# Kernel tuning notes

Measured on AMD Instinct MI355X. Metric: run time of the kernel, lower is better.

The kernel has to match this reference:

```python
import jax, jax.numpy as jnp
import numpy as np

N = 64      # SSM state size (hidden_size)
H = 1024    # channels
L = 2048    # sequence length
BATCH = 8


def setup_inputs() -> dict:
    key = jax.random.key(0)
    ks = jax.random.split(key, 12)
    s = 1.0 / np.sqrt(N)
    n = jnp.arange(N, dtype=jnp.float32)
    return {
        "r": jax.random.normal(ks[0], (BATCH, L, H), dtype=jnp.float32),
        "B_re": jax.random.normal(ks[1], (N,), dtype=jnp.float32) * s,
        "B_im": jax.random.normal(ks[2], (N,), dtype=jnp.float32) * s,
        "C_re": jax.random.normal(ks[3], (H, N), dtype=jnp.float32) * s,
        "C_im": jax.random.normal(ks[4], (H, N), dtype=jnp.float32) * s,
        "P_re": jax.random.normal(ks[5], (N,), dtype=jnp.float32) * s,
        "P_im": jax.random.normal(ks[6], (N,), dtype=jnp.float32) * s,
        "Q_re": jax.random.normal(ks[7], (N,), dtype=jnp.float32) * s,
        "Q_im": jax.random.normal(ks[8], (N,), dtype=jnp.float32) * s,
        # HiPPO-LegS-like diagonal: negative real part for stability, imag ~ pi*n
        "diag_re": -0.5 * jnp.ones((N,), dtype=jnp.float32),
        "diag_im": jnp.pi * (n - N / 2.0),
        "step": jnp.array([1e-3], dtype=jnp.float32),
        "D": jnp.zeros((1,), dtype=jnp.float32),
    }


def _dplr_kernel(Bc, Cc, Pc, Qc, Lam, step, seq_len):
    # Standard S4 DPLR generating function evaluated at roots of unity,
    # then inverse FFT -> real convolution kernel K_c of shape (H, L).
    z = jnp.exp(-2j * jnp.pi * jnp.arange(seq_len) / seq_len).astype(jnp.complex64)  # (L,)
    g = (2.0 / step) * (1.0 - z) / (1.0 + z)                                          # (L,)
    cden = 1.0 / (g[:, None] - Lam[None, :])                                          # (L,N) Cauchy denom
    k00 = jnp.einsum('hn,ln->hl', Cc * Bc, cden)   # (H,L)
    k01 = jnp.einsum('hn,ln->hl', Cc * Pc, cden)   # (H,L)
    k10 = jnp.einsum('n,ln->l', Qc * Bc, cden)     # (L,)
    k11 = jnp.einsum('n,ln->l', Qc * Pc, cden)     # (L,)
    at_roots = (2.0 / (1.0 + z)) * (k00 - k01 * (k10 / (1.0 + k11)))  # (H,L)
    return jnp.fft.ifft(at_roots, axis=-1).real


def reference(r, B_re, B_im, C_re, C_im, P_re, P_im, Q_re, Q_im,
              diag_re, diag_im, step, D):
    step_c = jnp.maximum(step[0], 1e-6)
    Bc = B_re + 1j * B_im
    Cc = C_re + 1j * C_im
    Pc = P_re + 1j * P_im
    Qc = Q_re + 1j * Q_im
    Lam = diag_re + 1j * diag_im
    seq_len = r.shape[1]
    K = _dplr_kernel(Bc, Cc, Pc, Qc, Lam, step_c, seq_len)  # (H, L)
    # causal FFT convolution along the sequence axis
    nfft = 2 * seq_len
    Kf = jnp.fft.rfft(K, n=nfft, axis=-1)            # (H, nfft//2+1)
    uf = jnp.fft.rfft(r, n=nfft, axis=1)             # (B, nfft//2+1, H)
    h1 = jnp.fft.irfft(uf * Kf.T[None], n=nfft, axis=1)[:, :seq_len]  # (B,L,H)
    y1 = h1 + D[0] * r
    return jax.nn.gelu(y1, approximate=False)
```

## Files before the change

kernel.cpp:

```cpp
#include <hip/hip_runtime.h>
#include <math.h>

#define SSM_N 64
#define SSM_H 1024
#define SSM_L 2048
#define SSM_B 8
#define FFTN 2048
#define NT 256
#define KFS 2052

#define PSWZ(a) ((a) ^ (((a) >> 4) & 15))

typedef float f2 __attribute__((ext_vector_type(2)));
static __device__ __forceinline__ f2 mkf2(float a, float b){ f2 v; v.x = a; v.y = b; return v; }

static __device__ __forceinline__ f2 cmul(f2 a, f2 b){
  return mkf2(-a.y, a.y) * mkf2(b.y, b.x) + mkf2(a.x, a.x) * b;
}
static __device__ __forceinline__ f2 cconj(f2 a){ return mkf2(a.x, -a.y); }

template<bool INV> static __device__ __forceinline__ f2 mul_mi(f2 a){
  return INV ? mkf2(-a.y, a.x) : mkf2(a.y, -a.x);
}
template<bool INV> static __device__ __forceinline__ f2 mul_w81(f2 a){
  const float r = 0.70710678118654752440f;
  return INV ? (r * mkf2(a.x - a.y, a.y + a.x)) : (r * mkf2(a.x + a.y, a.y - a.x));
}
template<bool INV> static __device__ __forceinline__ f2 mul_w83(f2 a){
  const float r = 0.70710678118654752440f;
  return INV ? (r * mkf2(-(a.x + a.y), a.x - a.y)) : (r * mkf2(a.y - a.x, -(a.x + a.y)));
}

template<bool INV>
static __device__ __forceinline__ void bfly8_store(f2* __restrict__ dst, const f2* __restrict__ tw,
                                                   f2* x, int j, int base, int S)
{
  f2 t0=x[0]+x[4], t4=x[0]-x[4];
  f2 t1=x[1]+x[5], t5=x[1]-x[5];
  f2 t2=x[2]+x[6], t6=x[2]-x[6];
  f2 t3=x[3]+x[7], t7=x[3]-x[7];
  f2 b0=t0+t2, b2=t0-t2, b1=t1+t3, b3=t1-t3;
  f2 mb3 = mul_mi<INV>(b3);
  f2 y0=b0+b1, y4=b0-b1, y2=b2+mb3, y6=b2-mb3;
  f2 v1 = mul_w81<INV>(t5), v2 = mul_mi<INV>(t6), v3 = mul_w83<INV>(t7);
  f2 a0=t4+v2, a2=t4-v2, a1=v1+v3, a3=v1-v3;
  f2 ma3 = mul_mi<INV>(a3);
  f2 y1=a0+a1, y5=a0-a1, y3=a2+ma3, y7=a2-ma3;
  f2 w1 = tw[j];
  if (INV) w1.y = -w1.y;
  f2 w2 = cmul(w1,w1);
  f2 w3 = cmul(w2,w1);
  f2 w4 = cmul(w2,w2);
  f2 w5 = cmul(w3,w2);
  f2 w6 = cmul(w3,w3);
  f2 w7 = cmul(w4,w3);
  dst[PSWZ(base)]     = y0;
  dst[PSWZ(base+S)]   = cmul(y1,w1);
  dst[PSWZ(base+2*S)] = cmul(y2,w2);
  dst[PSWZ(base+3*S)] = cmul(y3,w3);
  dst[PSWZ(base+4*S)] = cmul(y4,w4);
  dst[PSWZ(base+5*S)] = cmul(y5,w5);
  dst[PSWZ(base+6*S)] = cmul(y6,w6);
  dst[PSWZ(base+7*S)] = cmul(y7,w7);
}

template<bool INV, bool ZTOP>
static __device__ __forceinline__ void stage8_first(const f2* __restrict__ src, f2* __restrict__ dst,
                                                    const f2* __restrict__ tw, int t, int st)
{
  const f2* sp = src + st;
  f2 x[8];
  if (ZTOP) {
    #pragma unroll
    for (int q = 0; q < 4; ++q) { x[q] = sp[256*q]; x[q+4] = x[q]; }
    #pragma unroll
    for (int q = 0; q < 4; ++q) x[q+4] = mkf2(0.f, 0.f);
  } else {
    #pragma unroll
    for (int q = 0; q < 8; ++q) x[q] = sp[256*q];
  }
  bfly8_store<INV>(dst, tw, x, t, t*8, 1);
}

template<bool INV, int S>
static __device__ __forceinline__ void stage8_mid(const f2* __restrict__ src, f2* __restrict__ dst,
                                                  const f2* __restrict__ tw, int t, int st)
{
  const f2* sp = src + st;
  f2 x[8];
  #pragma unroll
  for (int q = 0; q < 8; ++q) x[q] = sp[256*q];
  int i = t & (S-1);
  int j = t - i;
  bfly8_store<INV>(dst, tw, x, j, i + j*8, S);
}

template<bool INV, bool HALFOUT>
static __device__ __forceinline__ void stage4f(const f2* __restrict__ src, f2* __restrict__ dst, int st)
{
  #pragma unroll
  for (int hh = 0; hh < 2; ++hh) {
    const f2* sp = src + st + 256*hh;
    f2* wp = dst + st + 256*hh;
    f2 x0=sp[0], x1=sp[512], x2=sp[1024], x3=sp[1536];
    f2 a0=x0+x2, a2=x0-x2, a1=x1+x3, a3=x1-x3;
    f2 m = mul_mi<INV>(a3);
    wp[0]   = a0+a1;
    wp[512] = a2+m;
    if (!HALFOUT) {
      wp[1024] = a0-a1;
      wp[1536] = a2-m;
    }
  }
}

template<bool INV, bool ZTOP, bool HALFOUT>
static __device__ void fft2048(f2* A, f2* B, const f2* tw, int t, int st)
{
  __syncthreads();
  stage8_first<INV, ZTOP>(A, B, tw, t, st);
  __syncthreads();
  stage8_mid<INV, 8>(B, A, tw, t, st);
  __syncthreads();
  stage8_mid<INV, 64>(A, B, tw, t, st);
  __syncthreads();
  stage4f<INV, HALFOUT>(B, A, st);
  __syncthreads();
}

static __device__ __forceinline__ void init_tw(f2* tw, int t)
{
  float s, c;
  sincosf(-6.2831853071795864769f * (float)t / (float)FFTN, &s, &c);
  tw[t] = mkf2(c, s);
}

__global__ __launch_bounds__(256) void kernel_cden(
    const float* __restrict__ B_re, const float* __restrict__ B_im,
    const float* __restrict__ P_re, const float* __restrict__ P_im,
    const float* __restrict__ Q_re, const float* __restrict__ Q_im,
    const float* __restrict__ diag_re, const float* __restrict__ diag_im,
    const float* __restrict__ step,
    f2* __restrict__ cdenT, f2* __restrict__ f2v, f2* __restrict__ facv)
{
  int l = blockIdx.x * blockDim.x + threadIdx.x;
  if (l >= SSM_L) return;
  double stepc = (double)step[0]; if (stepc < 1e-6) stepc = 1e-6;
  double ang = -2.0 * 3.14159265358979323846 * (double)l / (double)SSM_L;
  double zr = cos(ang), zi = sin(ang);
  double dr = 1.0 + zr, di = zi;
  double nr = 1.0 - zr, ni = -zi;
  double den = dr*dr + di*di;
  double i2s = 2.0 / stepc;
  double gr = i2s * (nr*dr + ni*di) / den;
  double gi = i2s * (ni*dr - nr*di) / den;
  f2v[l] = mkf2((float)(2.0*dr/den), (float)(-2.0*di/den));
  double k10r=0.0, k10i=0.0, k11r=0.0, k11i=0.0;
  for (int n = 0; n < SSM_N; ++n) {
    double ar = gr - (double)diag_re[n];
    double ai = gi - (double)diag_im[n];
    double d2 = ar*ar + ai*ai;
    double cr = ar/d2, ci = -ai/d2;
    cdenT[n*SSM_L + l] = mkf2((float)cr, (float)ci);
    double qr = (double)Q_re[n], qi = (double)Q_im[n];
    double br = (double)B_re[n], bi = (double)B_im[n];
    double pr = (double)P_re[n], pi = (double)P_im[n];
    double qbr = qr*br - qi*bi, qbi = qr*bi + qi*br;
    double qpr = qr*pr - qi*pi, qpi = qr*pi + qi*pr;
    k10r += qbr*cr - qbi*ci; k10i += qbr*ci + qbi*cr;
    k11r += qpr*cr - qpi*ci; k11i += qpr*ci + qpi*cr;
  }
  double er = 1.0 + k11r, ei = k11i;
  double ed = er*er + ei*ei;
  facv[l] = mkf2((float)((k10r*er + k10i*ei)/ed), (float)((k10i*er - k10r*ei)/ed));
}

__global__ __launch_bounds__(NT, 2) void kernel_khat(
    const float* __restrict__ C_re, const float* __restrict__ C_im,
    const float* __restrict__ B_re, const float* __restrict__ B_im,
    const float* __restrict__ P_re, const float* __restrict__ P_im,
    const f2* __restrict__ cdenT,
    const f2* __restrict__ f2v, const f2* __restrict__ facv,
    f2* __restrict__ Kf)
{
  __shared__ f2 bufA[FFTN];
  __shared__ f2 bufB[FFTN];
  __shared__ f2 tw[256];
  int t = threadIdx.x;
  int st = PSWZ(t);
  int h0 = blockIdx.x * 2;
  init_tw(tw, t);
  if (t < 128) {
    int h = h0 + (t >> 6), n = t & 63;
    f2 cc = mkf2(C_re[h*SSM_N + n], C_im[h*SSM_N + n]);
    bufA[t]       = cmul(cc, mkf2(B_re[n], B_im[n]));
    bufA[128 + t] = cmul(cc, mkf2(P_re[n], P_im[n]));
  }
  __syncthreads();
  f2 k00[2][8], k01[2][8];
  #pragma unroll
  for (int h = 0; h < 2; ++h)
    #pragma unroll
    for (int i = 0; i < 8; ++i) { k00[h][i] = mkf2(0.f,0.f); k01[h][i] = mkf2(0.f,0.f); }
  for (int n = 0; n < SSM_N; ++n) {
    f2 cd[8];
    #pragma unroll
    for (int i = 0; i < 8; ++i) cd[i] = cdenT[n*SSM_L + t + i*NT];
    #pragma unroll
    for (int h = 0; h < 2; ++h) {
      f2 cb = bufA[h*64 + n], cp = bufA[128 + h*64 + n];
      #pragma unroll
      for (int i = 0; i < 8; ++i) {
        k00[h][i] = k00[h][i] + cmul(cb, cd[i]);
        k01[h][i] = k01[h][i] + cmul(cp, cd[i]);
      }
    }
  }
  for (int h = 0; h < 2; ++h) {
    __syncthreads();
    #pragma unroll
    for (int i = 0; i < 8; ++i) {
      int l = t + i*NT;
      bufA[PSWZ(l)] = cmul(f2v[l], k00[h][i] - cmul(k01[h][i], facv[l]));
    }
    fft2048<true, false, false>(bufA, bufB, tw, t, st);
    const float scale = 1.0f / (float)FFTN;
    #pragma unroll
    for (int i = 0; i < 4; ++i) {
      int j = t + i*NT;
      bufB[PSWZ(j)] = mkf2(bufA[PSWZ(2*j)].x * scale, bufA[PSWZ(2*j+1)].x * scale);
    }
    fft2048<false, true, false>(bufB, bufA, tw, t, st);
    f2* krow = Kf + (size_t)(h0 + h) * KFS;
    #pragma unroll
    for (int i = 0; i < 4; ++i) {
      int k = t + i*NT;
      if (k == 0) {
        f2 c0 = bufB[0];
        krow[0]       = mkf2(c0.x + c0.y, 0.f);
        krow[FFTN]    = mkf2(c0.x - c0.y, 0.f);
        krow[FFTN/2]  = cconj(bufB[PSWZ(FFTN/2)]);
      } else {
        int kk = FFTN - k;
        f2 Ck = bufB[PSWZ(k)], Ckk = bufB[PSWZ(kk)];
        f2 E = mkf2(0.5f*(Ck.x + Ckk.x), 0.5f*(Ck.y - Ckk.y));
        f2 O = mkf2(0.5f*(Ck.y + Ckk.y), 0.5f*(Ckk.x - Ck.x));
        float s, c;
        sincosf(-3.14159265358979f * (float)k / (float)FFTN, &s, &c);
        krow[k]  = E + cmul(mkf2(c, s), O);
        krow[kk] = cconj(E) + cmul(mkf2(-c, s), cconj(O));
      }
    }
  }
}

__global__ __launch_bounds__(256) void ktranspose(const float* __restrict__ src, float* __restrict__ dst)
{
  __shared__ float tile[32][33];
  int tx = threadIdx.x & 31, ty = threadIdx.x >> 5;
  int h0 = blockIdx.x * 32, l0 = blockIdx.y * 32, b = blockIdx.z;
  const float* s = src + ((size_t)b*SSM_L + l0)*SSM_H + h0;
  #pragma unroll
  for (int i = 0; i < 4; ++i) { int row = ty + i*8; tile[row][tx] = s[(size_t)row*SSM_H + tx]; }
  __syncthreads();
  float* d = dst + ((size_t)b*SSM_H + h0)*SSM_L + l0;
  #pragma unroll
  for (int i = 0; i < 4; ++i) { int row = ty + i*8; d[(size_t)row*SSM_L + tx] = tile[tx][row]; }
}

__global__ __launch_bounds__(NT, 4) void kernel_conv(float* __restrict__ rT, const f2* __restrict__ Kf)
{
  __shared__ f2 bufA[FFTN];
  __shared__ f2 bufB[FFTN];
  __shared__ f2 tw[256];
  int t = threadIdx.x;
  int st = PSWZ(t);
  int row = blockIdx.x;
  int h = row & (SSM_H - 1);
  init_tw(tw, t);
  float* rrow = rT + (size_t)row * SSM_L;
  const float4* r4 = (const float4*)rrow;
  #pragma unroll
  for (int i = 0; i < 2; ++i) {
    int j2 = t + i*NT;
    float4 v = r4[j2];
    bufA[PSWZ(2*j2)]   = mkf2(v.x, v.y);
    bufA[PSWZ(2*j2+1)] = mkf2(v.z, v.w);
  }
  fft2048<false, true, false>(bufA, bufB, tw, t, st);
  const f2* krow = Kf + (size_t)h * KFS;
  #pragma unroll
  for (int i = 0; i < 4; ++i) {
    int k = t + i*NT;
    if (k == 0) {
      f2 c0 = bufA[0];
      float F0 = c0.x + c0.y, Fn = c0.x - c0.y;
      f2 K0 = krow[0], Kn = krow[FFTN];
      f2 G0 = F0 * K0;
      f2 Gn = Fn * Kn;
      f2 Xe = 0.5f * (G0 + Gn);
      f2 Xo = 0.5f * (G0 - Gn);
      bufB[0] = mkf2(Xe.x - Xo.y, Xe.y + Xo.x);
      f2 Gm = cmul(cconj(bufA[PSWZ(FFTN/2)]), krow[FFTN/2]);
      bufB[PSWZ(FFTN/2)] = cconj(Gm);
    } else {
      int kk = FFTN - k;
      f2 Ck = bufA[PSWZ(k)], Ckk = bufA[PSWZ(kk)];
      f2 E = mkf2(0.5f*(Ck.x + Ckk.x), 0.5f*(Ck.y - Ckk.y));
      f2 O = mkf2(0.5f*(Ck.y + Ckk.y), 0.5f*(Ckk.x - Ck.x));
      float s, c;
      sincosf(-3.14159265358979f * (float)k / (float)FFTN, &s, &c);
      f2 Fk  = E + cmul(mkf2(c, s), O);
      f2 Fkk = cconj(E) + cmul(mkf2(-c, s), cconj(O));
      f2 Gk  = cmul(Fk,  krow[k]);
      f2 Gkk = cmul(Fkk, krow[kk]);
      f2 Xe  = mkf2(0.5f*(Gk.x + Gkk.x), 0.5f*(Gk.y - Gkk.y));
      f2 Dd  = mkf2(0.5f*(Gk.x - Gkk.x), 0.5f*(Gk.y + Gkk.y));
      f2 Xo  = cmul(mkf2(c, -s), Dd);
      bufB[PSWZ(k)] = mkf2(Xe.x - Xo.y, Xe.y + Xo.x);
      f2 Xe2 = mkf2(0.5f*(Gkk.x + Gk.x), 0.5f*(Gkk.y - Gk.y));
      f2 Dd2 = mkf2(0.5f*(Gkk.x - Gk.x), 0.5f*(Gkk.y + Gk.y));
      f2 Xo2 = cmul(mkf2(-c, -s), Dd2);
      bufB[PSWZ(kk)] = mkf2(Xe2.x - Xo2.y, Xe2.y + Xo2.x);
    }
  }
  fft2048<true, false, true>(bufB, bufA, tw, t, st);
  const float sc = 1.0f / (float)FFTN;
  float4* w4 = (float4*)rrow;
  #pragma unroll
  for (int i = 0; i < 2; ++i) {
    int j2 = t + i*NT;
    f2 z0 = bufB[PSWZ(2*j2)], z1 = bufB[PSWZ(2*j2+1)];
    w4[j2] = make_float4(z0.x*sc, z0.y*sc, z1.x*sc, z1.y*sc);
  }
}

__global__ __launch_bounds__(256) void ktback(const float* __restrict__ yT, const float* __restrict__ r,
                                              const float* __restrict__ Dp, float* __restrict__ out)
{
  __shared__ float tile[32][33];
  int tx = threadIdx.x & 31, ty = threadIdx.x >> 5;
  int h0 = blockIdx.x * 32, l0 = blockIdx.y * 32, b = blockIdx.z;
  const float* s = yT + ((size_t)b*SSM_H + h0)*SSM_L + l0;
  #pragma unroll
  for (int i = 0; i < 4; ++i) { int row = ty + i*8; tile[row][tx] = s[(size_t)row*SSM_L + tx]; }
  __syncthreads();
  float Dv = Dp[0];
  float* o = out + ((size_t)b*SSM_L + l0)*SSM_H + h0;
  const float* rr = r + ((size_t)b*SSM_L + l0)*SSM_H + h0;
  #pragma unroll
  for (int i = 0; i < 4; ++i) {
    int row = ty + i*8;
    float x = tile[tx][row] + Dv * rr[(size_t)row*SSM_H + tx];
    float g = 0.5f * x * (1.0f + erff(x * 0.70710678118654752f));
    o[(size_t)row*SSM_H + tx] = g;
  }
}

extern "C" void kernel_launch(void* const* d_in, const int* in_sizes, int n_in,
                              void* d_out, int out_size, void* d_ws, size_t ws_size,
                              hipStream_t stream)
{
  const float* r       = (const float*)d_in[0];
  const float* B_re    = (const float*)d_in[1];
  const float* B_im    = (const float*)d_in[2];
  const float* C_re    = (const float*)d_in[3];
  const float* C_im    = (const float*)d_in[4];
  const float* P_re    = (const float*)d_in[5];
  const float* P_im    = (const float*)d_in[6];
  const float* Q_re    = (const float*)d_in[7];
  const float* Q_im    = (const float*)d_in[8];
  const float* diag_re = (const float*)d_in[9];
  const float* diag_im = (const float*)d_in[10];
  const float* step    = (const float*)d_in[11];
  const float* Dp      = (const float*)d_in[12];
  float* out = (float*)d_out;

  char* p = (char*)d_ws;
  float* rT  = (float*)p; p += (size_t)SSM_B*SSM_H*SSM_L*sizeof(float);
  f2* cdenT  = (f2*)p;    p += (size_t)SSM_N*SSM_L*sizeof(f2);
  f2* f2v    = (f2*)p;    p += (size_t)SSM_L*sizeof(f2);
  f2* facv   = (f2*)p;    p += (size_t)SSM_L*sizeof(f2);
  f2* Kf     = (f2*)p;    p += (size_t)SSM_H*KFS*sizeof(f2);

  kernel_cden<<<SSM_L/NT, NT, 0, stream>>>(B_re, B_im, P_re, P_im, Q_re, Q_im,
                                           diag_re, diag_im, step, cdenT, f2v, facv);
  kernel_khat<<<SSM_H/2, NT, 0, stream>>>(C_re, C_im, B_re, B_im, P_re, P_im,
                                          cdenT, f2v, facv, Kf);
  ktranspose<<<dim3(SSM_H/32, SSM_L/32, SSM_B), 256, 0, stream>>>(r, rT);
  kernel_conv<<<SSM_B*SSM_H, NT, 0, stream>>>(rT, Kf);
  ktback<<<dim3(SSM_H/32, SSM_L/32, SSM_B), 256, 0, stream>>>(rT, r, Dp, out);
}
```

Measured before the change: 312.3 us.

## Split kernel gen into GEMM+FFT, derive Kf analytically, widen transposes, fuse D skip

Splits the Cauchy/GEMM stage from the FFT stage: a kgemm kernel writes the at-roots values to workspace, and a one-row-per-block kfft kernel recovers the real kernel with one inverse FFT. Odd rfft bins come from one twisted forward FFT, and even bins are computed directly from the at-roots values, replacing the second full FFT. The cden kernel now splits the N sum across 8 lanes and reduces with shuffles. Transposes use 64x64 tiles with float4 loads and stores, the D*r skip term moves into the conv kernel, and per-element sincos calls are replaced by one base twiddle times constant eighth-roots. This adds a workspace round trip for the at-roots data and reuses the rT buffer before the transpose overwrites it.

```diff
diff --git a/kernel.cpp b/kernel.cpp
--- a/kernel.cpp
+++ b/kernel.cpp
@@ -30,6 +30,23 @@
   const float r = 0.70710678118654752440f;
   return INV ? (r * mkf2(-(a.x + a.y), a.x - a.y)) : (r * mkf2(a.y - a.x, -(a.x + a.y)));
 }
+
+#define W8C0 1.f
+#define W8S0 0.f
+#define W8C1 0.92387953251f
+#define W8S1 (-0.38268343236f)
+#define W8C2 0.70710678119f
+#define W8S2 (-0.70710678119f)
+#define W8C3 0.38268343236f
+#define W8S3 (-0.92387953251f)
+#define W8C4 0.f
+#define W8S4 (-1.f)
+#define W8C5 (-0.38268343236f)
+#define W8S5 (-0.92387953251f)
+#define W8C6 (-0.70710678119f)
+#define W8S6 (-0.70710678119f)
+#define W8C7 (-0.92387953251f)
+#define W8S7 (-0.38268343236f)
 
 template<bool INV>
 static __device__ __forceinline__ void bfly8_store(f2* __restrict__ dst, const f2* __restrict__ tw,
@@ -72,9 +89,7 @@
   f2 x[8];
   if (ZTOP) {
     #pragma unroll
-    for (int q = 0; q < 4; ++q) { x[q] = sp[256*q]; x[q+4] = x[q]; }
-    #pragma unroll
-    for (int q = 0; q < 4; ++q) x[q+4] = mkf2(0.f, 0.f);
+    for (int q = 0; q < 4; ++q) { x[q] = sp[256*q]; x[q+4] = mkf2(0.f, 0.f); }
   } else {
     #pragma unroll
     for (int q = 0; q < 8; ++q) x[q] = sp[256*q];
@@ -143,8 +158,8 @@
     const float* __restrict__ step,
     f2* __restrict__ cdenT, f2* __restrict__ f2v, f2* __restrict__ facv)
 {
-  int l = blockIdx.x * blockDim.x + threadIdx.x;
-  if (l >= SSM_L) return;
+  int gid = blockIdx.x * blockDim.x + threadIdx.x;
+  int l = gid >> 3, s = gid & 7;
   double stepc = (double)step[0]; if (stepc < 1e-6) stepc = 1e-6;
   double ang = -2.0 * 3.14159265358979323846 * (double)l / (double)SSM_L;
   double zr = cos(ang), zi = sin(ang);
@@ -154,9 +169,10 @@
   double i2s = 2.0 / stepc;
   double gr = i2s * (nr*dr + ni*di) / den;
   double gi = i2s * (ni*dr - nr*di) / den;
-  f2v[l] = mkf2((float)(2.0*dr/den), (float)(-2.0*di/den));
   double k10r=0.0, k10i=0.0, k11r=0.0, k11i=0.0;
-  for (int n = 0; n < SSM_N; ++n) {
+  #pragma unroll
+  for (int q = 0; q < 8; ++q) {
+    int n = s*8 + q;
     double ar = gr - (double)diag_re[n];
     double ai = gi - (double)diag_im[n];
     double d2 = ar*ar + ai*ai;
@@ -170,105 +186,144 @@
     k10r += qbr*cr - qbi*ci; k10i += qbr*ci + qbi*cr;
     k11r += qpr*cr - qpi*ci; k11i += qpr*ci + qpi*cr;
   }
-  double er = 1.0 + k11r, ei = k11i;
-  double ed = er*er + ei*ei;
-  facv[l] = mkf2((float)((k10r*er + k10i*ei)/ed), (float)((k10i*er - k10r*ei)/ed));
-}
-
-__global__ __launch_bounds__(NT, 2) void kernel_khat(
+  #pragma unroll
+  for (int off = 1; off < 8; off <<= 1) {
+    k10r += __shfl_xor(k10r, off);
+    k10i += __shfl_xor(k10i, off);
+    k11r += __shfl_xor(k11r, off);
+    k11i += __shfl_xor(k11i, off);
+  }
+  if (s == 0) {
+    f2v[l] = mkf2((float)(2.0*dr/den), (float)(-2.0*di/den));
+    double er = 1.0 + k11r, ei = k11i;
+    double ed = er*er + ei*ei;
+    facv[l] = mkf2((float)((k10r*er + k10i*ei)/ed), (float)((k10i*er - k10r*ei)/ed));
+  }
+}
+
+__global__ __launch_bounds__(NT, 2) void kgemm(
     const float* __restrict__ C_re, const float* __restrict__ C_im,
     const float* __restrict__ B_re, const float* __restrict__ B_im,
     const float* __restrict__ P_re, const float* __restrict__ P_im,
-    const f2* __restrict__ cdenT,
-    const f2* __restrict__ f2v, const f2* __restrict__ facv,
-    f2* __restrict__ Kf)
+    const f2* __restrict__ cdenT, const f2* __restrict__ f2v, const f2* __restrict__ facv,
+    f2* __restrict__ atr)
+{
+  __shared__ f2 cbs[256];
+  int t = threadIdx.x;
+  int h0 = blockIdx.x * 2;
+  if (t < 128) {
+    int h = h0 + (t >> 6), n = t & 63;
+    f2 cc = mkf2(C_re[h*SSM_N + n], C_im[h*SSM_N + n]);
+    cbs[t]       = cmul(cc, mkf2(B_re[n], B_im[n]));
+    cbs[128 + t] = cmul(cc, mkf2(P_re[n], P_im[n]));
+  }
+  __syncthreads();
+  f2 k00[2][8], k01[2][8];
+  #pragma unroll
+  for (int h = 0; h < 2; ++h)
+    #pragma unroll
+    for (int i = 0; i < 8; ++i) { k00[h][i] = mkf2(0.f,0.f); k01[h][i] = mkf2(0.f,0.f); }
+  for (int n = 0; n < SSM_N; ++n) {
+    f2 cd[8];
+    #pragma unroll
+    for (int i = 0; i < 8; ++i) cd[i] = cdenT[n*SSM_L + t + i*NT];
+    #pragma unroll
+    for (int h = 0; h < 2; ++h) {
+      f2 cb = cbs[h*64 + n], cp = cbs[128 + h*64 + n];
+      #pragma unroll
+      for (int i = 0; i < 8; ++i) {
+        k00[h][i] = k00[h][i] + cmul(cb, cd[i]);
+        k01[h][i] = k01[h][i] + cmul(cp, cd[i]);
+      }
+    }
+  }
+  #pragma unroll
+  for (int h = 0; h < 2; ++h) {
+    f2* arow = atr + (size_t)(h0 + h) * SSM_L;
+    #pragma unroll
+    for (int i = 0; i < 8; ++i) {
+      int l = t + i*NT;
+      arow[l] = cmul(f2v[l], k00[h][i] - cmul(k01[h][i], facv[l]));
+    }
+  }
+}
+
+__global__ __launch_bounds__(NT, 4) void kfft(const f2* __restrict__ atr, f2* __restrict__ Kf)
 {
   __shared__ f2 bufA[FFTN];
   __shared__ f2 bufB[FFTN];
   __shared__ f2 tw[256];
   int t = threadIdx.x;
   int st = PSWZ(t);
-  int h0 = blockIdx.x * 2;
+  int h = blockIdx.x;
   init_tw(tw, t);
-  if (t < 128) {
-    int h = h0 + (t >> 6), n = t & 63;
-    f2 cc = mkf2(C_re[h*SSM_N + n], C_im[h*SSM_N + n]);
-    bufA[t]       = cmul(cc, mkf2(B_re[n], B_im[n]));
-    bufA[128 + t] = cmul(cc, mkf2(P_re[n], P_im[n]));
-  }
-  __syncthreads();
-  f2 k00[2][8], k01[2][8];
-  #pragma unroll
-  for (int h = 0; h < 2; ++h)
-    #pragma unroll
-    for (int i = 0; i < 8; ++i) { k00[h][i] = mkf2(0.f,0.f); k01[h][i] = mkf2(0.f,0.f); }
-  for (int n = 0; n < SSM_N; ++n) {
-    f2 cd[8];
-    #pragma unroll
-    for (int i = 0; i < 8; ++i) cd[i] = cdenT[n*SSM_L + t + i*NT];
-    #pragma unroll
-    for (int h = 0; h < 2; ++h) {
-      f2 cb = bufA[h*64 + n], cp = bufA[128 + h*64 + n];
-      #pragma unroll
-      for (int i = 0; i < 8; ++i) {
-        k00[h][i] = k00[h][i] + cmul(cb, cd[i]);
-        k01[h][i] = k01[h][i] + cmul(cp, cd[i]);
-      }
-    }
-  }
-  for (int h = 0; h < 2; ++h) {
-    __syncthreads();
+  const f2* arow = atr + (size_t)h * SSM_L;
+  #pragma unroll
+  for (int i = 0; i < 8; ++i) {
+    int n = t + i*NT;
+    bufA[PSWZ(n)] = arow[n];
+  }
+  fft2048<true, false, false>(bufA, bufB, tw, t, st);
+  float sb, cb;
+  sincosf(-3.14159265358979f * (float)t / (float)FFTN, &sb, &cb);
+  f2 base = mkf2(cb, sb);
+  const float scale = 1.0f / (float)FFTN;
+  {
+    const float Wc[8] = {W8C0,W8C1,W8C2,W8C3,W8C4,W8C5,W8C6,W8C7};
+    const float Ws[8] = {W8S0,W8S1,W8S2,W8S3,W8S4,W8S5,W8S6,W8S7};
     #pragma unroll
     for (int i = 0; i < 8; ++i) {
-      int l = t + i*NT;
-      bufA[PSWZ(l)] = cmul(f2v[l], k00[h][i] - cmul(k01[h][i], facv[l]));
-    }
-    fft2048<true, false, false>(bufA, bufB, tw, t, st);
-    const float scale = 1.0f / (float)FFTN;
-    #pragma unroll
-    for (int i = 0; i < 4; ++i) {
-      int j = t + i*NT;
-      bufB[PSWZ(j)] = mkf2(bufA[PSWZ(2*j)].x * scale, bufA[PSWZ(2*j+1)].x * scale);
-    }
-    fft2048<false, true, false>(bufB, bufA, tw, t, st);
-    f2* krow = Kf + (size_t)(h0 + h) * KFS;
-    #pragma unroll
-    for (int i = 0; i < 4; ++i) {
-      int k = t + i*NT;
-      if (k == 0) {
-        f2 c0 = bufB[0];
-        krow[0]       = mkf2(c0.x + c0.y, 0.f);
-        krow[FFTN]    = mkf2(c0.x - c0.y, 0.f);
-        krow[FFTN/2]  = cconj(bufB[PSWZ(FFTN/2)]);
-      } else {
-        int kk = FFTN - k;
-        f2 Ck = bufB[PSWZ(k)], Ckk = bufB[PSWZ(kk)];
-        f2 E = mkf2(0.5f*(Ck.x + Ckk.x), 0.5f*(Ck.y - Ckk.y));
-        f2 O = mkf2(0.5f*(Ck.y + Ckk.y), 0.5f*(Ckk.x - Ck.x));
-        float s, c;
-        sincosf(-3.14159265358979f * (float)k / (float)FFTN, &s, &c);
-        krow[k]  = E + cmul(mkf2(c, s), O);
-        krow[kk] = cconj(E) + cmul(mkf2(-c, s), cconj(O));
-      }
+      int n = t + i*NT;
+      float K = bufA[PSWZ(n)].x * scale;
+      f2 c = cmul(base, mkf2(Wc[i], Ws[i]));
+      bufB[PSWZ(n)] = K * c;
+    }
+  }
+  fft2048<false, false, true>(bufB, bufA, tw, t, st);
+  f2* krow = Kf + (size_t)h * KFS;
+  #pragma unroll
+  for (int i = 0; i < 4; ++i) {
+    int m = t + i*NT;
+    krow[2*m+1] = bufB[PSWZ(m)];
+  }
+  #pragma unroll
+  for (int i = 0; i < 4; ++i) {
+    int m = t + i*NT;
+    if (m == 0) {
+      krow[0]    = mkf2(arow[0].x, 0.f);
+      krow[FFTN] = mkf2(arow[FFTN/2].x, 0.f);
+    } else {
+      krow[2*m] = 0.5f * (arow[m] + cconj(arow[FFTN - m]));
     }
   }
 }
 
 __global__ __launch_bounds__(256) void ktranspose(const float* __restrict__ src, float* __restrict__ dst)
 {
-  __shared__ float tile[32][33];
-  int tx = threadIdx.x & 31, ty = threadIdx.x >> 5;
-  int h0 = blockIdx.x * 32, l0 = blockIdx.y * 32, b = blockIdx.z;
-  const float* s = src + ((size_t)b*SSM_L + l0)*SSM_H + h0;
-  #pragma unroll
-  for (int i = 0; i < 4; ++i) { int row = ty + i*8; tile[row][tx] = s[(size_t)row*SSM_H + tx]; }
-  __syncthreads();
-  float* d = dst + ((size_t)b*SSM_H + h0)*SSM_L + l0;
-  #pragma unroll
-  for (int i = 0; i < 4; ++i) { int row = ty + i*8; d[(size_t)row*SSM_L + tx] = tile[tx][row]; }
-}
-
-__global__ __launch_bounds__(NT, 4) void kernel_conv(float* __restrict__ rT, const f2* __restrict__ Kf)
+  __shared__ float til[64][65];
+  int t = threadIdx.x, tx = t & 15, ty = t >> 4;
+  int h0 = blockIdx.x * 64, l0 = blockIdx.y * 64, b = blockIdx.z;
+  const float4* s4 = (const float4*)(src + ((size_t)b*SSM_L + l0)*SSM_H + h0);
+  #pragma unroll
+  for (int i = 0; i < 4; ++i) {
+    int lr = ty + 16*i;
+    float4 v = s4[(size_t)lr*(SSM_H/4) + tx];
+    til[lr][4*tx+0]=v.x; til[lr][4*tx+1]=v.y; til[lr][4*tx+2]=v.z; til[lr][4*tx+3]=v.w;
+  }
+  __syncthreads();
+  float4* d4 = (float4*)(dst + ((size_t)b*SSM_H + h0)*SSM_L + l0);
+  #pragma unroll
+  for (int i = 0; i < 4; ++i) {
+    int hr = ty + 16*i;
+    float4 w;
+    w.x = til[4*tx+0][hr]; w.y = til[4*tx+1][hr];
+    w.z = til[4*tx+2][hr]; w.w = til[4*tx+3][hr];
+    d4[(size_t)hr*(SSM_L/4) + tx] = w;
+  }
+}
+
+__global__ __launch_bounds__(NT, 4) void kernel_conv(float* __restrict__ rT, const f2* __restrict__ Kf,
+                                                     const float* __restrict__ Dp)
 {
   __shared__ f2 bufA[FFTN];
   __shared__ f2 bufB[FFTN];
@@ -277,51 +332,60 @@
   int st = PSWZ(t);
   int row = blockIdx.x;
   int h = row & (SSM_H - 1);
+  float Dv = Dp[0];
   init_tw(tw, t);
   float* rrow = rT + (size_t)row * SSM_L;
   const float4* r4 = (const float4*)rrow;
+  float4 vin[2];
   #pragma unroll
   for (int i = 0; i < 2; ++i) {
     int j2 = t + i*NT;
-    float4 v = r4[j2];
-    bufA[PSWZ(2*j2)]   = mkf2(v.x, v.y);
-    bufA[PSWZ(2*j2+1)] = mkf2(v.z, v.w);
+    vin[i] = r4[j2];
+    bufA[PSWZ(2*j2)]   = mkf2(vin[i].x, vin[i].y);
+    bufA[PSWZ(2*j2+1)] = mkf2(vin[i].z, vin[i].w);
   }
   fft2048<false, true, false>(bufA, bufB, tw, t, st);
   const f2* krow = Kf + (size_t)h * KFS;
-  #pragma unroll
-  for (int i = 0; i < 4; ++i) {
-    int k = t + i*NT;
-    if (k == 0) {
-      f2 c0 = bufA[0];
-      float F0 = c0.x + c0.y, Fn = c0.x - c0.y;
-      f2 K0 = krow[0], Kn = krow[FFTN];
-      f2 G0 = F0 * K0;
-      f2 Gn = Fn * Kn;
-      f2 Xe = 0.5f * (G0 + Gn);
-      f2 Xo = 0.5f * (G0 - Gn);
-      bufB[0] = mkf2(Xe.x - Xo.y, Xe.y + Xo.x);
-      f2 Gm = cmul(cconj(bufA[PSWZ(FFTN/2)]), krow[FFTN/2]);
-      bufB[PSWZ(FFTN/2)] = cconj(Gm);
-    } else {
-      int kk = FFTN - k;
-      f2 Ck = bufA[PSWZ(k)], Ckk = bufA[PSWZ(kk)];
-      f2 E = mkf2(0.5f*(Ck.x + Ckk.x), 0.5f*(Ck.y - Ckk.y));
-      f2 O = mkf2(0.5f*(Ck.y + Ckk.y), 0.5f*(Ckk.x - Ck.x));
-      float s, c;
-      sincosf(-3.14159265358979f * (float)k / (float)FFTN, &s, &c);
-      f2 Fk  = E + cmul(mkf2(c, s), O);
-      f2 Fkk = cconj(E) + cmul(mkf2(-c, s), cconj(O));
-      f2 Gk  = cmul(Fk,  krow[k]);
-      f2 Gkk = cmul(Fkk, krow[kk]);
-      f2 Xe  = mkf2(0.5f*(Gk.x + Gkk.x), 0.5f*(Gk.y - Gkk.y));
-      f2 Dd  = mkf2(0.5f*(Gk.x - Gkk.x), 0.5f*(Gk.y + Gkk.y));
-      f2 Xo  = cmul(mkf2(c, -s), Dd);
-      bufB[PSWZ(k)] = mkf2(Xe.x - Xo.y, Xe.y + Xo.x);
-      f2 Xe2 = mkf2(0.5f*(Gkk.x + Gk.x), 0.5f*(Gkk.y - Gk.y));
-      f2 Dd2 = mkf2(0.5f*(Gkk.x - Gk.x), 0.5f*(Gkk.y + Gk.y));
-      f2 Xo2 = cmul(mkf2(-c, -s), Dd2);
-      bufB[PSWZ(kk)] = mkf2(Xe2.x - Xo2.y, Xe2.y + Xo2.x);
+  float sb, cb;
+  sincosf(-3.14159265358979f * (float)t / (float)FFTN, &sb, &cb);
+  f2 base = mkf2(cb, sb);
+  {
+    const float Wc[4] = {W8C0,W8C1,W8C2,W8C3};
+    const float Ws[4] = {W8S0,W8S1,W8S2,W8S3};
+    #pragma unroll
+    for (int i = 0; i < 4; ++i) {
+      int k = t + i*NT;
+      f2 w = cmul(base, mkf2(Wc[i], Ws[i]));
+      float c = w.x, s = w.y;
+      if (k == 0) {
+        f2 c0 = bufA[0];
+        float F0 = c0.x + c0.y, Fn = c0.x - c0.y;
+        f2 K0 = krow[0], Kn = krow[FFTN];
+        f2 G0 = F0 * K0;
+        f2 Gn = Fn * Kn;
+        f2 Xe = 0.5f * (G0 + Gn);
+        f2 Xo = 0.5f * (G0 - Gn);
+        bufB[0] = mkf2(Xe.x - Xo.y, Xe.y + Xo.x);
+        f2 Gm = cmul(cconj(bufA[PSWZ(FFTN/2)]), krow[FFTN/2]);
+        bufB[PSWZ(FFTN/2)] = cconj(Gm);
+      } else {
+        int kk = FFTN - k;
+        f2 Ck = bufA[PSWZ(k)], Ckk = bufA[PSWZ(kk)];
+        f2 E = mkf2(0.5f*(Ck.x + Ckk.x), 0.5f*(Ck.y - Ckk.y));
+        f2 O = mkf2(0.5f*(Ck.y + Ckk.y), 0.5f*(Ckk.x - Ck.x));
+        f2 Fk  = E + cmul(mkf2(c, s), O);
+        f2 Fkk = cconj(E) + cmul(mkf2(-c, s), cconj(O));
+        f2 Gk  = cmul(Fk,  krow[k]);
+        f2 Gkk = cmul(Fkk, krow[kk]);
+        f2 Xe  = mkf2(0.5f*(Gk.x + Gkk.x), 0.5f*(Gk.y - Gkk.y));
+        f2 Dd  = mkf2(0.5f*(Gk.x - Gkk.x), 0.5f*(Gk.y + Gkk.y));
+        f2 Xo  = cmul(mkf2(c, -s), Dd);
+        bufB[PSWZ(k)] = mkf2(Xe.x - Xo.y, Xe.y + Xo.x);
+        f2 Xe2 = mkf2(0.5f*(Gkk.x + Gk.x), 0.5f*(Gkk.y - Gk.y));
+        f2 Dd2 = mkf2(0.5f*(Gkk.x - Gk.x), 0.5f*(Gkk.y + Gk.y));
+        f2 Xo2 = cmul(mkf2(-c, -s), Dd2);
+        bufB[PSWZ(kk)] = mkf2(Xe2.x - Xo2.y, Xe2.y + Xo2.x);
+      }
     }
   }
   fft2048<true, false, true>(bufB, bufA, tw, t, st);
@@ -331,29 +395,36 @@
   for (int i = 0; i < 2; ++i) {
     int j2 = t + i*NT;
     f2 z0 = bufB[PSWZ(2*j2)], z1 = bufB[PSWZ(2*j2+1)];
-    w4[j2] = make_float4(z0.x*sc, z0.y*sc, z1.x*sc, z1.y*sc);
-  }
-}
-
-__global__ __launch_bounds__(256) void ktback(const float* __restrict__ yT, const float* __restrict__ r,
-                                              const float* __restrict__ Dp, float* __restrict__ out)
-{
-  __shared__ float tile[32][33];
-  int tx = threadIdx.x & 31, ty = threadIdx.x >> 5;
-  int h0 = blockIdx.x * 32, l0 = blockIdx.y * 32, b = blockIdx.z;
-  const float* s = yT + ((size_t)b*SSM_H + h0)*SSM_L + l0;
-  #pragma unroll
-  for (int i = 0; i < 4; ++i) { int row = ty + i*8; tile[row][tx] = s[(size_t)row*SSM_L + tx]; }
-  __syncthreads();
-  float Dv = Dp[0];
-  float* o = out + ((size_t)b*SSM_L + l0)*SSM_H + h0;
-  const float* rr = r + ((size_t)b*SSM_L + l0)*SSM_H + h0;
-  #pragma unroll
-  for (int i = 0; i < 4; ++i) {
-    int row = ty + i*8;
-    float x = tile[tx][row] + Dv * rr[(size_t)row*SSM_H + tx];
-    float g = 0.5f * x * (1.0f + erff(x * 0.70710678118654752f));
-    o[(size_t)row*SSM_H + tx] = g;
+    w4[j2] = make_float4(z0.x*sc + Dv*vin[i].x, z0.y*sc + Dv*vin[i].y,
+                         z1.x*sc + Dv*vin[i].z, z1.y*sc + Dv*vin[i].w);
+  }
+}
+
+__global__ __launch_bounds__(256) void ktback(const float* __restrict__ yT, float* __restrict__ out)
+{
+  __shared__ float til[64][65];
+  int t = threadIdx.x, tx = t & 15, ty = t >> 4;
+  int h0 = blockIdx.x * 64, l0 = blockIdx.y * 64, b = blockIdx.z;
+  const float4* s4 = (const float4*)(yT + ((size_t)b*SSM_H + h0)*SSM_L + l0);
+  #pragma unroll
+  for (int i = 0; i < 4; ++i) {
+    int hr = ty + 16*i;
+    float4 v = s4[(size_t)hr*(SSM_L/4) + tx];
+    til[hr][4*tx+0]=v.x; til[hr][4*tx+1]=v.y; til[hr][4*tx+2]=v.z; til[hr][4*tx+3]=v.w;
+  }
+  __syncthreads();
+  float4* d4 = (float4*)(out + ((size_t)b*SSM_L + l0)*SSM_H + h0);
+  #pragma unroll
+  for (int i = 0; i < 4; ++i) {
+    int lr = ty + 16*i;
+    float4 w;
+    float x0 = til[4*tx+0][lr], x1 = til[4*tx+1][lr];
+    float x2 = til[4*tx+2][lr], x3 = til[4*tx+3][lr];
+    w.x = 0.5f * x0 * (1.0f + erff(x0 * 0.70710678118654752f));
+    w.y = 0.5f * x1 * (1.0f + erff(x1 * 0.70710678118654752f));
+    w.z = 0.5f * x2 * (1.0f + erff(x2 * 0.70710678118654752f));
+    w.w = 0.5f * x3 * (1.0f + erff(x3 * 0.70710678118654752f));
+    d4[(size_t)lr*(SSM_H/4) + tx] = w;
   }
 }
 
@@ -382,12 +453,14 @@
   f2* f2v    = (f2*)p;    p += (size_t)SSM_L*sizeof(f2);
   f2* facv   = (f2*)p;    p += (size_t)SSM_L*sizeof(f2);
   f2* Kf     = (f2*)p;    p += (size_t)SSM_H*KFS*sizeof(f2);
-
-  kernel_cden<<<SSM_L/NT, NT, 0, stream>>>(B_re, B_im, P_re, P_im, Q_re, Q_im,
-                                           diag_re, diag_im, step, cdenT, f2v, facv);
-  kernel_khat<<<SSM_H/2, NT, 0, stream>>>(C_re, C_im, B_re, B_im, P_re, P_im,
-                                          cdenT, f2v, facv, Kf);
-  ktranspose<<<dim3(SSM_H/32, SSM_L/32, SSM_B), 256, 0, stream>>>(r, rT);
-  kernel_conv<<<SSM_B*SSM_H, NT, 0, stream>>>(rT, Kf);
-  ktback<<<dim3(SSM_H/32, SSM_L/32, SSM_B), 256, 0, stream>>>(rT, r, Dp, out);
-}
+  f2* atr = (f2*)rT;
+
+  kernel_cden<<<SSM_L*8/NT, NT, 0, stream>>>(B_re, B_im, P_re, P_im, Q_re, Q_im,
+                                             diag_re, diag_im, step, cdenT, f2v, facv);
+  kgemm<<<SSM_H/2, NT, 0, stream>>>(C_re, C_im, B_re, B_im, P_re, P_im,
+                                    cdenT, f2v, facv, atr);
+  kfft<<<SSM_H, NT, 0, stream>>>(atr, Kf);
+  ktranspose<<<dim3(SSM_H/64, SSM_L/64, SSM_B), 256, 0, stream>>>(r, rT);
+  kernel_conv<<<SSM_B*SSM_H, NT, 0, stream>>>(rT, Kf, Dp);
+  ktback<<<dim3(SSM_H/64, SSM_L/64, SSM_B), 256, 0, stream>>>(rT, out);
+}
```

New measurement: 287.3 us. -8.0%, faster.
